# Optimization experiments

Measured on AMD Instinct MI355X. Metric: run time of the kernel, lower is better.

Reference implementation:

```python
import jax, jax.numpy as jnp
import numpy as np

P = 8          # patch_size = window_size // 3
C = 3          # in_channel (forced to 3 by the module's reshape logic)
QK_SCALE = 1.0


def _rel_bias(p):
    """Fixed relative-position bias [9, p, p], matching the torch constructor."""
    i = np.arange(p, dtype=np.float64)
    down = np.exp(-i / (p / 2))[:, None] * np.ones((1, p))   # down[i, :] = exp(-i/(p/2))
    right = down.T
    br = np.exp(-(i[:, None] + i[None, :]) / (p / 2))        # symmetric exp(-(i+j)/(p/2))
    merge = np.stack([
        np.rot90(br, 2), np.flip(down, 0), np.rot90(br, 1),
        np.flip(right, 1), np.ones((p, p)), right,
        np.rot90(br, 3), down, br,
    ], axis=0)
    return jnp.asarray(merge, dtype=jnp.float32)


def setup_inputs() -> dict:
    key = jax.random.key(0)
    k1, k2, k3 = jax.random.split(key, 3)
    b, c, h, w = 8, C, 512, 512
    d = c * P * P  # 192
    x = jax.random.normal(k1, (b, c, h, w), jnp.float32)
    W_qkv = jax.random.normal(k2, (3 * d, d), jnp.float32) * 0.05  # torch Linear weight [out, in]
    b_qkv = jax.random.normal(k3, (3 * d,), jnp.float32) * 0.01
    return {"x": x, "W_qkv": W_qkv, "b_qkv": b_qkv}


def reference(x, W_qkv, b_qkv):
    p, c = P, C
    b, _, h, w = x.shape
    nh, nw = h // p, w // p
    # pad by one patch on each side (zeros)
    xp = jnp.pad(x, ((0, 0), (0, 0), (p, p), (p, p)))
    # patch grid: [b, c, nh+2, p, nw+2, p] -> [b, nh+2, nw+2, c, p, p]
    g = xp.reshape(b, c, nh + 2, p, nw + 2, p).transpose(0, 2, 4, 1, 3, 5)
    # 9 neighbor patches per window, index k = 3*di + dj (row-major over 3x3 blocks)
    neigh = jnp.stack(
        [g[:, di:di + nh, dj:dj + nw] for di in range(3) for dj in range(3)],
        axis=3,
    )  # [b, nh, nw, 9, c, p, p]
    feat = neigh.reshape(b, nh, nw, 9, c * p * p)
    # qkv linear: y = feat @ W^T + b
    qkv = jnp.einsum('bijnd,ed->bijne', feat, W_qkv) + b_qkv  # [b, nh, nw, 9, 3*c*p*p]
    qkv = qkv.reshape(b, nh, nw, 9, 3, c, p, p)
    q = qkv[..., 0, :, :, :]  # [b, nh, nw, 9, c, p, p]
    k = qkv[..., 1, :, :, :]
    v = qkv[..., 2, :, :, :]
    core_q = q[:, :, :, 4] * QK_SCALE          # center patch query [b, nh, nw, c, p, p]
    bias = _rel_bias(p)                        # [9, p, p]
    # elementwise attention: (q * k * bias) * v, summed over the 9-neighbor window
    attn = core_q[:, :, :, None] * k * bias[:, None]   # [b, nh, nw, 9, c, p, p]
    out = jnp.sum(attn * v, axis=3)                    # [b, nh, nw, c, p, p]
    # reassemble to image: [b, c, nh, p, nw, p] -> [b, c, h, w]
    return out.transpose(0, 3, 1, 4, 2, 5).reshape(b, c, nh * p, nw * p)
```

## Files before the change

kernel.cpp:

```cpp
#include <hip/hip_runtime.h>


#define HW 512
#define PLANE 6291456

typedef __attribute__((ext_vector_type(8))) short bf16x8;
typedef __attribute__((ext_vector_type(4))) float f32x4;

static __device__ __forceinline__ unsigned short bf16_rne(float f) {
    unsigned u = __builtin_bit_cast(unsigned, f);
    u += 0x7FFFu + ((u >> 16) & 1u);
    return (unsigned short)(u >> 16);
}
static __device__ __forceinline__ float bf16f(unsigned short h) {
    unsigned u = ((unsigned)h) << 16;
    return __builtin_bit_cast(float, u);
}

__global__ void __launch_bounds__(256) wprep_kernel(const float* __restrict__ W,
                                                    unsigned short* __restrict__ Ws)
{
    int gid = blockIdx.x * 256 + threadIdx.x;
    int k4  = gid & 15;
    int t   = gid >> 4;
    int er  = t % 192;
    int ckt = t / 192;
    int c   = ckt / 3, kt = ckt % 3;
    int k0  = k4 << 2;
    int slot = er >> 6, dl = er & 63;
    const float* src = W + (size_t)(slot*192 + c*64 + dl)*192 + kt*64 + k0;
    float4 v = *(const float4*)src;
    unsigned short h0 = bf16_rne(v.x), h1 = bf16_rne(v.y), h2 = bf16_rne(v.z), h3 = bf16_rne(v.w);
    unsigned short l0 = bf16_rne(v.x - bf16f(h0)), l1 = bf16_rne(v.y - bf16f(h1)),
                   l2 = bf16_rne(v.z - bf16f(h2)), l3 = bf16_rne(v.w - bf16f(h3));
    int unit = (k0 >> 3) ^ (er & 7);
    size_t off = (size_t)ckt*24576 + (size_t)er*64 + unit*8 + (k0 & 7);
    *(uint2*)(Ws + off)         = make_uint2((unsigned)h0 | ((unsigned)h1 << 16),
                                             (unsigned)h2 | ((unsigned)h3 << 16));
    *(uint2*)(Ws + off + 12288) = make_uint2((unsigned)l0 | ((unsigned)l1 << 16),
                                             (unsigned)l2 | ((unsigned)l3 << 16));
}

__global__ void __launch_bounds__(256) qkv_mfma_kernel(
    const float* __restrict__ x,
    const unsigned short* __restrict__ Ws,
    const float* __restrict__ bqkv,
    float* __restrict__ ws)
{
    __shared__ char smem[65536];
    unsigned short* Ah = (unsigned short*)smem;
    unsigned short* Al = Ah + 4096;

    const int tid = threadIdx.x;
    const int mb  = blockIdx.x;
    const int c   = blockIdx.y;
    const int b   = mb >> 6, i = mb & 63;
    const int wv  = tid >> 6;
    const int l   = tid & 63;
    const int lr  = l & 15;
    const int lk  = l >> 4;

    f32x4 acc[4][3];
    #pragma unroll
    for (int m = 0; m < 4; ++m)
        #pragma unroll
        for (int n = 0; n < 3; ++n)
            #pragma unroll
            for (int r = 0; r < 4; ++r) acc[m][n][r] = 0.f;

    for (int kt = 0; kt < 3; ++kt) {
        const float4* xs = (const float4*)(x + ((size_t)(b*3 + kt)*HW + (size_t)i*8) * HW);
        #pragma unroll
        for (int it = 0; it < 4; ++it) {
            int f  = tid + it*256;
            float4 a = xs[f];
            int pi = f >> 7;
            int m_ = f & 127;
            int j  = m_ >> 1;
            int k  = pi*8 + ((m_ & 1) << 2);
            unsigned short h0 = bf16_rne(a.x), h1 = bf16_rne(a.y), h2 = bf16_rne(a.z), h3 = bf16_rne(a.w);
            unsigned short q0 = bf16_rne(a.x - bf16f(h0)), q1 = bf16_rne(a.y - bf16f(h1)),
                           q2 = bf16_rne(a.z - bf16f(h2)), q3 = bf16_rne(a.w - bf16f(h3));
            int byte = (j*128 + k*2) ^ ((j & 7) << 4);
            *(uint2*)((char*)Ah + byte) = make_uint2((unsigned)h0 | ((unsigned)h1 << 16),
                                                     (unsigned)h2 | ((unsigned)h3 << 16));
            *(uint2*)((char*)Al + byte) = make_uint2((unsigned)q0 | ((unsigned)q1 << 16),
                                                     (unsigned)q2 | ((unsigned)q3 << 16));
        }
        {
            const uint4* bsrc = (const uint4*)(Ws + (size_t)(c*3 + kt)*24576);
            uint4* bdst = (uint4*)(smem + 16384);
            #pragma unroll
            for (int it = 0; it < 12; ++it) bdst[tid + it*256] = bsrc[tid + it*256];
        }
        __syncthreads();

        #pragma unroll
        for (int ks = 0; ks < 2; ++ks) {
            const int kb = (ks*32 + lk*8) * 2;
            bf16x8 ahf[4], alf[4], bhf[3], blf[3];
            #pragma unroll
            for (int m = 0; m < 4; ++m) {
                int row = m*16 + lr;
                int byte = (row*128 + kb) ^ ((row & 7) << 4);
                ahf[m] = *(const bf16x8*)((const char*)Ah + byte);
                alf[m] = *(const bf16x8*)((const char*)Al + byte);
            }
            #pragma unroll
            for (int n = 0; n < 3; ++n) {
                int er = wv*48 + n*16 + lr;
                int byte = (er*128 + kb) ^ ((er & 7) << 4);
                bhf[n] = *(const bf16x8*)(smem + 16384 + byte);
                blf[n] = *(const bf16x8*)(smem + 40960 + byte);
            }
            #pragma unroll
            for (int m = 0; m < 4; ++m)
                #pragma unroll
                for (int n = 0; n < 3; ++n) {
                    acc[m][n] = __builtin_amdgcn_mfma_f32_16x16x32_bf16(alf[m], bhf[n], acc[m][n], 0, 0, 0);
                    acc[m][n] = __builtin_amdgcn_mfma_f32_16x16x32_bf16(ahf[m], blf[n], acc[m][n], 0, 0, 0);
                    acc[m][n] = __builtin_amdgcn_mfma_f32_16x16x32_bf16(ahf[m], bhf[n], acc[m][n], 0, 0, 0);
                }
        }
        __syncthreads();
    }

    float* qt  = (float*)smem;
    float* ktl = qt + 4352;
    float* vtl = ktl + 4352;
    #pragma unroll
    for (int n = 0; n < 3; ++n) {
        int er = wv*48 + n*16 + lr;
        int slot = er >> 6, dl = er & 63;
        float bias = bqkv[slot*192 + c*64 + dl];
        float* tile = (slot == 0) ? qt : (slot == 1) ? ktl : vtl;
        #pragma unroll
        for (int m = 0; m < 4; ++m)
            #pragma unroll
            for (int ri = 0; ri < 4; ++ri) {
                int j = m*16 + lk*4 + ri;
                tile[j*68 + dl] = acc[m][n][ri] + bias;
            }
    }
    __syncthreads();

    float* qplane = ws;
    float* wplane = ws + PLANE;
    size_t pixbase = ((size_t)(b*3 + c)*HW + (size_t)i*8) * HW;
    #pragma unroll
    for (int it = 0; it < 4; ++it) {
        int f  = tid + it*256;
        int pi = f >> 7;
        int m_ = f & 127;
        int j  = m_ >> 1;
        int dl = pi*8 + ((m_ & 1) << 2);
        float4 q4 = *(float4*)&qt[j*68 + dl];
        float4 k4 = *(float4*)&ktl[j*68 + dl];
        float4 v4 = *(float4*)&vtl[j*68 + dl];
        size_t off = pixbase + (size_t)pi*HW + m_*4;
        *(float4*)(qplane + off) = q4;
        float4 w4;
        w4.x = k4.x*v4.x; w4.y = k4.y*v4.y; w4.z = k4.z*v4.z; w4.w = k4.w*v4.w;
        *(float4*)(wplane + off) = w4;
    }
}

__global__ void __launch_bounds__(256) attn_kernel(
    const float* __restrict__ ws,
    const float* __restrict__ bqkv,
    float* __restrict__ out)
{
    __shared__ float wt[80][84];
    const int tid = threadIdx.x;
    int bid = blockIdx.x;
    int txt = (bid & 7) << 6;
    int tyt = ((bid >> 3) & 7) << 6;
    int pl  = bid >> 6;
    int c   = pl % 3;
    const float* qplane = ws + (size_t)pl * (HW*HW);
    const float* wplane = ws + PLANE + (size_t)pl * (HW*HW);

    for (int it = 0; it < 7; ++it) {
        int f = tid + it*256;
        if (f < 1600) {
            int r  = f / 20;
            int c4 = f - r*20;
            int gy = tyt - 8 + r;
            int gx = txt - 8 + (c4 << 2);
            float4 v;
            if ((unsigned)gy < 512u && (unsigned)gx < 512u) {
                v = *(const float4*)(wplane + (size_t)gy*HW + gx);
            } else {
                int d0 = c*64 + (gy & 7)*8 + (gx & 7);
                float4 bk = *(const float4*)(bqkv + 192 + d0);
                float4 bv = *(const float4*)(bqkv + 384 + d0);
                v.x = bk.x*bv.x; v.y = bk.y*bv.y; v.z = bk.z*bv.z; v.w = bk.w*bv.w;
            }
            *(float4*)&wt[r][c4 << 2] = v;
        }
    }
    __syncthreads();

    #pragma unroll
    for (int it = 0; it < 4; ++it) {
        int f  = tid + it*256;
        int ly = f >> 4;
        int lx = (f & 15) << 2;
        int pi = ly & 7, pj0 = lx & 7;
        float fr0 = __expf((float)(pi - 7) * 0.25f);
        float fr2 = __expf((float)(-pi) * 0.25f);
        float fa[4], fb[4];
        #pragma unroll
        for (int u = 0; u < 4; ++u) {
            int pj = pj0 + u;
            fa[u] = __expf((float)(pj - 7) * 0.25f);
            fb[u] = __expf((float)(-pj) * 0.25f);
        }
        float sx = 0.f, sy = 0.f, sz = 0.f, sw = 0.f;
        #pragma unroll
        for (int di = 0; di < 3; ++di) {
            const float* row = &wt[ly + 8*di][lx];
            float4 w0 = *(const float4*)(row);
            float4 w1 = *(const float4*)(row + 8);
            float4 w2 = *(const float4*)(row + 16);
            float fr = (di == 0) ? fr0 : (di == 1) ? 1.f : fr2;
            sx += fr * (fa[0]*w0.x + w1.x + fb[0]*w2.x);
            sy += fr * (fa[1]*w0.y + w1.y + fb[1]*w2.y);
            sz += fr * (fa[2]*w0.z + w1.z + fb[2]*w2.z);
            sw += fr * (fa[3]*w0.w + w1.w + fb[3]*w2.w);
        }
        size_t off = (size_t)pl*(HW*HW) + (size_t)(tyt + ly)*HW + txt + lx;
        float4 q4 = *(const float4*)(qplane + (size_t)(tyt + ly)*HW + txt + lx);
        float4 o;
        o.x = q4.x*sx; o.y = q4.y*sy; o.z = q4.z*sz; o.w = q4.w*sw;
        *(float4*)(out + off) = o;
    }
}

extern "C" void kernel_launch(void* const* d_in, const int* in_sizes, int n_in,
                              void* d_out, int out_size, void* d_ws, size_t ws_size,
                              hipStream_t stream)
{
    const float* x  = (const float*)d_in[0];
    const float* W  = (const float*)d_in[1];
    const float* bq = (const float*)d_in[2];
    float* wsf = (float*)d_ws;
    unsigned short* Wsplit = (unsigned short*)(wsf + 2*(size_t)PLANE);

    wprep_kernel<<<108, 256, 0, stream>>>(W, Wsplit);
    qkv_mfma_kernel<<<dim3(512, 3), 256, 0, stream>>>(x, Wsplit, bq, wsf);
    attn_kernel<<<1536, 256, 0, stream>>>(wsf, bq, (float*)d_out);
}
```

Baseline: 123.3 us.

## Pre-split x into bf16 hi/lo planes and load MFMA fragments directly from global

Adds a separate kernel that converts x into bf16 high/low planes, and relayouts the split weights so the QKV kernel loads its MFMA fragments straight from global memory without staging through LDS or using block barriers. The epilogue now writes q and k*v directly from the accumulators, after remapping the output columns so each wave owns matching q/k/v columns. This drops the shared-memory tile and transpose. In the attention kernel the exp bias factors are hoisted out of the loop. The cost is an extra pass over x that writes and re-reads 2x bf16 data, plus scattered 4-byte global stores in the epilogue.

```diff
diff --git a/kernel.cpp b/kernel.cpp
--- a/kernel.cpp
+++ b/kernel.cpp
@@ -17,40 +17,75 @@
     return __builtin_bit_cast(float, u);
 }
 
+__global__ void __launch_bounds__(256) xsplit_kernel(
+    const float* __restrict__ x,
+    unsigned short* __restrict__ xh,
+    unsigned short* __restrict__ xl)
+{
+    int gid = blockIdx.x * 256 + threadIdx.x;
+    const float4* s = (const float4*)x + (size_t)gid * 2;
+    float4 a = s[0], b = s[1];
+    float v[8] = {a.x, a.y, a.z, a.w, b.x, b.y, b.z, b.w};
+    unsigned short h[8], lo[8];
+    #pragma unroll
+    for (int u = 0; u < 8; ++u) {
+        h[u]  = bf16_rne(v[u]);
+        lo[u] = bf16_rne(v[u] - bf16f(h[u]));
+    }
+    uint4 hp, lp;
+    hp.x = (unsigned)h[0] | ((unsigned)h[1] << 16);
+    hp.y = (unsigned)h[2] | ((unsigned)h[3] << 16);
+    hp.z = (unsigned)h[4] | ((unsigned)h[5] << 16);
+    hp.w = (unsigned)h[6] | ((unsigned)h[7] << 16);
+    lp.x = (unsigned)lo[0] | ((unsigned)lo[1] << 16);
+    lp.y = (unsigned)lo[2] | ((unsigned)lo[3] << 16);
+    lp.z = (unsigned)lo[4] | ((unsigned)lo[5] << 16);
+    lp.w = (unsigned)lo[6] | ((unsigned)lo[7] << 16);
+    ((uint4*)xh)[gid] = hp;
+    ((uint4*)xl)[gid] = lp;
+}
+
 __global__ void __launch_bounds__(256) wprep_kernel(const float* __restrict__ W,
                                                     unsigned short* __restrict__ Ws)
 {
     int gid = blockIdx.x * 256 + threadIdx.x;
-    int k4  = gid & 15;
-    int t   = gid >> 4;
-    int er  = t % 192;
-    int ckt = t / 192;
-    int c   = ckt / 3, kt = ckt % 3;
-    int k0  = k4 << 2;
+    int er  = gid % 192;
+    int t   = gid / 192;
+    int kg  = t & 7;
+    int ckt = t >> 3;
+    int c = ckt / 3, kt = ckt % 3;
     int slot = er >> 6, dl = er & 63;
-    const float* src = W + (size_t)(slot*192 + c*64 + dl)*192 + kt*64 + k0;
-    float4 v = *(const float4*)src;
-    unsigned short h0 = bf16_rne(v.x), h1 = bf16_rne(v.y), h2 = bf16_rne(v.z), h3 = bf16_rne(v.w);
-    unsigned short l0 = bf16_rne(v.x - bf16f(h0)), l1 = bf16_rne(v.y - bf16f(h1)),
-                   l2 = bf16_rne(v.z - bf16f(h2)), l3 = bf16_rne(v.w - bf16f(h3));
-    int unit = (k0 >> 3) ^ (er & 7);
-    size_t off = (size_t)ckt*24576 + (size_t)er*64 + unit*8 + (k0 & 7);
-    *(uint2*)(Ws + off)         = make_uint2((unsigned)h0 | ((unsigned)h1 << 16),
-                                             (unsigned)h2 | ((unsigned)h3 << 16));
-    *(uint2*)(Ws + off + 12288) = make_uint2((unsigned)l0 | ((unsigned)l1 << 16),
-                                             (unsigned)l2 | ((unsigned)l3 << 16));
+    const float* src = W + (size_t)(slot*192 + c*64 + dl)*192 + kt*64 + kg*8;
+    float4 a = ((const float4*)src)[0], b = ((const float4*)src)[1];
+    float v[8] = {a.x, a.y, a.z, a.w, b.x, b.y, b.z, b.w};
+    unsigned short h[8], lo[8];
+    #pragma unroll
+    for (int u = 0; u < 8; ++u) {
+        h[u]  = bf16_rne(v[u]);
+        lo[u] = bf16_rne(v[u] - bf16f(h[u]));
+    }
+    uint4 hp, lp;
+    hp.x = (unsigned)h[0] | ((unsigned)h[1] << 16);
+    hp.y = (unsigned)h[2] | ((unsigned)h[3] << 16);
+    hp.z = (unsigned)h[4] | ((unsigned)h[5] << 16);
+    hp.w = (unsigned)h[6] | ((unsigned)h[7] << 16);
+    lp.x = (unsigned)lo[0] | ((unsigned)lo[1] << 16);
+    lp.y = (unsigned)lo[2] | ((unsigned)lo[3] << 16);
+    lp.z = (unsigned)lo[4] | ((unsigned)lo[5] << 16);
+    lp.w = (unsigned)lo[6] | ((unsigned)lo[7] << 16);
+    size_t oh = ((size_t)((ckt*2 + 0)*8 + kg)*192 + er) * 8;
+    size_t ol = ((size_t)((ckt*2 + 1)*8 + kg)*192 + er) * 8;
+    *(uint4*)(Ws + oh) = hp;
+    *(uint4*)(Ws + ol) = lp;
 }
 
 __global__ void __launch_bounds__(256) qkv_mfma_kernel(
-    const float* __restrict__ x,
+    const unsigned short* __restrict__ xh,
+    const unsigned short* __restrict__ xl,
     const unsigned short* __restrict__ Ws,
     const float* __restrict__ bqkv,
     float* __restrict__ ws)
 {
-    __shared__ char smem[65536];
-    unsigned short* Ah = (unsigned short*)smem;
-    unsigned short* Al = Ah + 4096;
-
     const int tid = threadIdx.x;
     const int mb  = blockIdx.x;
     const int c   = blockIdx.y;
@@ -68,101 +103,60 @@
             #pragma unroll
             for (int r = 0; r < 4; ++r) acc[m][n][r] = 0.f;
 
+    #pragma unroll
     for (int kt = 0; kt < 3; ++kt) {
-        const float4* xs = (const float4*)(x + ((size_t)(b*3 + kt)*HW + (size_t)i*8) * HW);
-        #pragma unroll
-        for (int it = 0; it < 4; ++it) {
-            int f  = tid + it*256;
-            float4 a = xs[f];
-            int pi = f >> 7;
-            int m_ = f & 127;
-            int j  = m_ >> 1;
-            int k  = pi*8 + ((m_ & 1) << 2);
-            unsigned short h0 = bf16_rne(a.x), h1 = bf16_rne(a.y), h2 = bf16_rne(a.z), h3 = bf16_rne(a.w);
-            unsigned short q0 = bf16_rne(a.x - bf16f(h0)), q1 = bf16_rne(a.y - bf16f(h1)),
-                           q2 = bf16_rne(a.z - bf16f(h2)), q3 = bf16_rne(a.w - bf16f(h3));
-            int byte = (j*128 + k*2) ^ ((j & 7) << 4);
-            *(uint2*)((char*)Ah + byte) = make_uint2((unsigned)h0 | ((unsigned)h1 << 16),
-                                                     (unsigned)h2 | ((unsigned)h3 << 16));
-            *(uint2*)((char*)Al + byte) = make_uint2((unsigned)q0 | ((unsigned)q1 << 16),
-                                                     (unsigned)q2 | ((unsigned)q3 << 16));
-        }
-        {
-            const uint4* bsrc = (const uint4*)(Ws + (size_t)(c*3 + kt)*24576);
-            uint4* bdst = (uint4*)(smem + 16384);
-            #pragma unroll
-            for (int it = 0; it < 12; ++it) bdst[tid + it*256] = bsrc[tid + it*256];
-        }
-        __syncthreads();
-
+        const unsigned short* xhp = xh + ((size_t)(b*3 + kt)*HW + (size_t)i*8) * HW;
+        const unsigned short* xlp = xl + ((size_t)(b*3 + kt)*HW + (size_t)i*8) * HW;
+        const unsigned short* Bb  = Ws + (size_t)(c*3 + kt) * 2 * 8 * 192 * 8;
         #pragma unroll
         for (int ks = 0; ks < 2; ++ks) {
-            const int kb = (ks*32 + lk*8) * 2;
-            bf16x8 ahf[4], alf[4], bhf[3], blf[3];
+            const int pi = ks*4 + lk;
+            bf16x8 ah[4], al[4];
             #pragma unroll
             for (int m = 0; m < 4; ++m) {
-                int row = m*16 + lr;
-                int byte = (row*128 + kb) ^ ((row & 7) << 4);
-                ahf[m] = *(const bf16x8*)((const char*)Ah + byte);
-                alf[m] = *(const bf16x8*)((const char*)Al + byte);
+                int j = m*16 + lr;
+                size_t o = (size_t)pi*HW + j*8;
+                ah[m] = *(const bf16x8*)(xhp + o);
+                al[m] = *(const bf16x8*)(xlp + o);
             }
+            bf16x8 bh[3], bl[3];
             #pragma unroll
             for (int n = 0; n < 3; ++n) {
-                int er = wv*48 + n*16 + lr;
-                int byte = (er*128 + kb) ^ ((er & 7) << 4);
-                bhf[n] = *(const bf16x8*)(smem + 16384 + byte);
-                blf[n] = *(const bf16x8*)(smem + 40960 + byte);
+                int er = n*64 + wv*16 + lr;
+                size_t oh = ((size_t)(0*8 + ks*4 + lk)*192 + er) * 8;
+                size_t ol = ((size_t)(1*8 + ks*4 + lk)*192 + er) * 8;
+                bh[n] = *(const bf16x8*)(Bb + oh);
+                bl[n] = *(const bf16x8*)(Bb + ol);
             }
             #pragma unroll
             for (int m = 0; m < 4; ++m)
                 #pragma unroll
                 for (int n = 0; n < 3; ++n) {
-                    acc[m][n] = __builtin_amdgcn_mfma_f32_16x16x32_bf16(alf[m], bhf[n], acc[m][n], 0, 0, 0);
-                    acc[m][n] = __builtin_amdgcn_mfma_f32_16x16x32_bf16(ahf[m], blf[n], acc[m][n], 0, 0, 0);
-                    acc[m][n] = __builtin_amdgcn_mfma_f32_16x16x32_bf16(ahf[m], bhf[n], acc[m][n], 0, 0, 0);
+                    acc[m][n] = __builtin_amdgcn_mfma_f32_16x16x32_bf16(al[m], bh[n], acc[m][n], 0, 0, 0);
+                    acc[m][n] = __builtin_amdgcn_mfma_f32_16x16x32_bf16(ah[m], bl[n], acc[m][n], 0, 0, 0);
+                    acc[m][n] = __builtin_amdgcn_mfma_f32_16x16x32_bf16(ah[m], bh[n], acc[m][n], 0, 0, 0);
                 }
         }
-        __syncthreads();
-    }
-
-    float* qt  = (float*)smem;
-    float* ktl = qt + 4352;
-    float* vtl = ktl + 4352;
-    #pragma unroll
-    for (int n = 0; n < 3; ++n) {
-        int er = wv*48 + n*16 + lr;
-        int slot = er >> 6, dl = er & 63;
-        float bias = bqkv[slot*192 + c*64 + dl];
-        float* tile = (slot == 0) ? qt : (slot == 1) ? ktl : vtl;
-        #pragma unroll
-        for (int m = 0; m < 4; ++m)
-            #pragma unroll
-            for (int ri = 0; ri < 4; ++ri) {
-                int j = m*16 + lk*4 + ri;
-                tile[j*68 + dl] = acc[m][n][ri] + bias;
-            }
-    }
-    __syncthreads();
-
+    }
+
+    const int dl = wv*16 + lr;
+    const float bq = bqkv[      c*64 + dl];
+    const float bk = bqkv[192 + c*64 + dl];
+    const float bv = bqkv[384 + c*64 + dl];
+    const int ppi = dl >> 3, ppj = dl & 7;
     float* qplane = ws;
     float* wplane = ws + PLANE;
-    size_t pixbase = ((size_t)(b*3 + c)*HW + (size_t)i*8) * HW;
-    #pragma unroll
-    for (int it = 0; it < 4; ++it) {
-        int f  = tid + it*256;
-        int pi = f >> 7;
-        int m_ = f & 127;
-        int j  = m_ >> 1;
-        int dl = pi*8 + ((m_ & 1) << 2);
-        float4 q4 = *(float4*)&qt[j*68 + dl];
-        float4 k4 = *(float4*)&ktl[j*68 + dl];
-        float4 v4 = *(float4*)&vtl[j*68 + dl];
-        size_t off = pixbase + (size_t)pi*HW + m_*4;
-        *(float4*)(qplane + off) = q4;
-        float4 w4;
-        w4.x = k4.x*v4.x; w4.y = k4.y*v4.y; w4.z = k4.z*v4.z; w4.w = k4.w*v4.w;
-        *(float4*)(wplane + off) = w4;
-    }
+    size_t rowoff = ((size_t)(b*3 + c)*HW + (size_t)(i*8 + ppi))*HW + ppj;
+    #pragma unroll
+    for (int m = 0; m < 4; ++m)
+        #pragma unroll
+        for (int ri = 0; ri < 4; ++ri) {
+            int j = m*16 + lk*4 + ri;
+            float qv = acc[m][0][ri] + bq;
+            float wvv = (acc[m][1][ri] + bk) * (acc[m][2][ri] + bv);
+            qplane[rowoff + (size_t)j*8] = qv;
+            wplane[rowoff + (size_t)j*8] = wvv;
+        }
 }
 
 __global__ void __launch_bounds__(256) attn_kernel(
@@ -179,6 +173,18 @@
     int c   = pl % 3;
     const float* qplane = ws + (size_t)pl * (HW*HW);
     const float* wplane = ws + PLANE + (size_t)pl * (HW*HW);
+
+    const int pi  = (tid >> 4) & 7;
+    const int pj0 = (tid & 1) << 2;
+    const float fr0 = __expf((float)(pi - 7) * 0.25f);
+    const float fr2 = __expf((float)(-pi) * 0.25f);
+    float fa[4], fb[4];
+    #pragma unroll
+    for (int u = 0; u < 4; ++u) {
+        int pj = pj0 + u;
+        fa[u] = __expf((float)(pj - 7) * 0.25f);
+        fb[u] = __expf((float)(-pj) * 0.25f);
+    }
 
     for (int it = 0; it < 7; ++it) {
         int f = tid + it*256;
@@ -206,16 +212,6 @@
         int f  = tid + it*256;
         int ly = f >> 4;
         int lx = (f & 15) << 2;
-        int pi = ly & 7, pj0 = lx & 7;
-        float fr0 = __expf((float)(pi - 7) * 0.25f);
-        float fr2 = __expf((float)(-pi) * 0.25f);
-        float fa[4], fb[4];
-        #pragma unroll
-        for (int u = 0; u < 4; ++u) {
-            int pj = pj0 + u;
-            fa[u] = __expf((float)(pj - 7) * 0.25f);
-            fb[u] = __expf((float)(-pj) * 0.25f);
-        }
         float sx = 0.f, sy = 0.f, sz = 0.f, sw = 0.f;
         #pragma unroll
         for (int di = 0; di < 3; ++di) {
@@ -245,9 +241,12 @@
     const float* W  = (const float*)d_in[1];
     const float* bq = (const float*)d_in[2];
     float* wsf = (float*)d_ws;
-    unsigned short* Wsplit = (unsigned short*)(wsf + 2*(size_t)PLANE);
-
-    wprep_kernel<<<108, 256, 0, stream>>>(W, Wsplit);
-    qkv_mfma_kernel<<<dim3(512, 3), 256, 0, stream>>>(x, Wsplit, bq, wsf);
+    unsigned short* xh = (unsigned short*)(wsf + 2*(size_t)PLANE);
+    unsigned short* xl = xh + PLANE;
+    unsigned short* Wsplit = xl + PLANE;
+
+    xsplit_kernel<<<3072, 256, 0, stream>>>(x, xh, xl);
+    wprep_kernel<<<54, 256, 0, stream>>>(W, Wsplit);
+    qkv_mfma_kernel<<<dim3(512, 3), 256, 0, stream>>>(xh, xl, Wsplit, bq, wsf);
     attn_kernel<<<1536, 256, 0, stream>>>(wsf, bq, (float*)d_out);
 }
```

Result: no change. 123.6 us (+0.2%).
